# Kernel tuning notes

Hardware: AMD Instinct MI355X
Metric: run time of the kernel (lower is better)

The kernel has to match this reference:

```python
import jax, jax.numpy as jnp
import numpy as np

B, L, H, M = 8, 512, 768, 383
N = M + 1  # +1 dummy epsilon mention
NEG = -10000.0


def _lin(x, W, b):
    return x @ W.T + b


def setup_inputs() -> dict:
    key = jax.random.key(0)
    ks = jax.random.split(key, 26)
    s = 0.02
    inp = {}
    inp["sequence_output"] = jax.random.normal(ks[0], (B, L, H), jnp.float32)
    inp["speaker_emb"] = jax.random.normal(ks[1], (400, H), jnp.float32) * s
    inp["dummy_emb"] = jax.random.normal(ks[2], (1, H), jnp.float32) * s
    inp["W_pair1"] = jax.random.normal(ks[3], (H, 2 * H), jnp.float32) * s
    inp["b_pair1"] = jnp.zeros((H,), jnp.float32)
    inp["W_pair2"] = jax.random.normal(ks[4], (H // 2, H), jnp.float32) * s
    inp["b_pair2"] = jnp.zeros((H // 2,), jnp.float32)
    inp["W_pair3"] = jax.random.normal(ks[5], (1, H // 2), jnp.float32) * s
    inp["b_pair3"] = jnp.zeros((1,), jnp.float32)
    inp["W_m1"] = jax.random.normal(ks[6], (H // 2, H), jnp.float32) * s
    inp["b_m1"] = jnp.zeros((H // 2,), jnp.float32)
    inp["W_m2"] = jax.random.normal(ks[7], (H // 4, H // 2), jnp.float32) * s
    inp["b_m2"] = jnp.zeros((H // 4,), jnp.float32)
    inp["W_m3"] = jax.random.normal(ks[8], (1, H // 4), jnp.float32) * s
    inp["b_m3"] = jnp.zeros((1,), jnp.float32)
    inp["W_c1"] = jax.random.normal(ks[9], (H // 2, H), jnp.float32) * s
    inp["b_c1"] = jnp.zeros((H // 2,), jnp.float32)
    inp["W_c2"] = jax.random.normal(ks[10], (18, H // 2), jnp.float32) * s
    inp["b_c2"] = jnp.zeros((18,), jnp.float32)
    inp["mentions_seg"] = jax.random.randint(ks[11], (M,), 0, B, jnp.int32)
    inp["mention_start"] = jax.random.randint(ks[12], (M,), 0, L, jnp.int32)
    inp["mention_end"] = jax.random.randint(ks[13], (M,), 0, L, jnp.int32)
    inp["speaker_ids"] = jax.random.randint(ks[14], (B, L), 0, 400, jnp.int32)
    second = jnp.arange(1, N, dtype=jnp.int32)  # each real mention is a 'second' exactly once
    first = jax.random.randint(ks[15], (M,), 0, N, jnp.int32) % second  # antecedent strictly before
    inp["link_first"] = first
    inp["link_second"] = second
    inp["character_label"] = jax.random.randint(ks[16], (M,), 0, 18, jnp.int32)
    return inp


def reference(sequence_output, speaker_emb, dummy_emb,
              W_pair1, b_pair1, W_pair2, b_pair2, W_pair3, b_pair3,
              W_m1, b_m1, W_m2, b_m2, W_m3, b_m3,
              W_c1, b_c1, W_c2, b_c2,
              mentions_seg, mention_start, mention_end, speaker_ids,
              link_first, link_second, character_label):
    relu = jax.nn.relu
    # gather mention boundary + speaker reps: [M, H]
    start_rep = sequence_output[mentions_seg, mention_start]
    end_rep = sequence_output[mentions_seg, mention_end]
    spk_rep = speaker_emb[speaker_ids[mentions_seg, mention_start]]
    mention_reps = start_rep + end_rep + spk_rep
    # character linking head: [M, 18]
    char_logits = _lin(relu(_lin(mention_reps, W_c1, b_c1)), W_c2, b_c2)
    # prepend dummy epsilon mention: [N, H]
    all_reps = jnp.concatenate([dummy_emb, mention_reps], axis=0)
    # pairwise MLP; pair[i, j] = MLP(cat(rep_j, rep_i)). Split W_pair1 to avoid [N,N,2H] concat.
    Wa, Wb = W_pair1[:, :H], W_pair1[:, H:]
    A = all_reps @ Wa.T  # contribution of 'first' (column j)
    Bm = all_reps @ Wb.T  # contribution of 'second' (row i)
    h1 = relu(A[None, :, :] + Bm[:, None, :] + b_pair1)  # [N, N, H]
    h2 = relu(jnp.einsum('ijk,hk->ijh', h1, W_pair2) + b_pair2)  # [N, N, H/2]
    pair_scores = jnp.einsum('ijh,oh->ij', h2, W_pair3) + b_pair3[0]  # [N, N]
    # unary mention score: [N]
    ms = (_lin(relu(_lin(relu(_lin(all_reps, W_m1, b_m1)), W_m2, b_m2)), W_m3, b_m3))[:, 0]
    mask = jnp.triu(jnp.ones((N, N), jnp.float32), k=0) * NEG
    mention_scores = pair_scores + ms[None, :] + ms[:, None] + mask
    # linking loss via row-softmax and link gathers
    sm = jax.nn.softmax(mention_scores, axis=1)
    lik = sm[link_second, link_first]  # [num_links]
    col_sum = jnp.zeros((N,), sm.dtype).at[link_second].add(lik)
    nll = -jnp.sum(jnp.log(col_sum[1:]))
    # character cross-entropy (sum reduction)
    logp = jax.nn.log_softmax(char_logits, axis=1)
    ce = -jnp.sum(jnp.take_along_axis(logp, character_label[:, None], axis=1))
    return nll + ce


if __name__ == '__main__':
    out = reference(**setup_inputs())
    print(out)
```

## Files before the change

### kernel.cpp

```cpp
#include <hip/hip_runtime.h>

typedef __bf16 bf16x8 __attribute__((ext_vector_type(8)));
typedef float f32x4 __attribute__((ext_vector_type(4)));

#define WS_ALLREPS 0
#define WS_APRIME  294912
#define WS_BMAT    589824
#define WS_RELUM1  884736
#define WS_RELUC1  1032192
#define WS_MS      1179648
#define WS_W2BF    1180032
#define WS_S       1327488

#define SWZ(row,c) (((row)<<2) + ((c) ^ (((row)>>1)&3)))

__device__ __forceinline__ bf16x8 cvt8(float4 a, float4 b) {
  bf16x8 v;
  v[0]=(__bf16)a.x; v[1]=(__bf16)a.y; v[2]=(__bf16)a.z; v[3]=(__bf16)a.w;
  v[4]=(__bf16)b.x; v[5]=(__bf16)b.y; v[6]=(__bf16)b.z; v[7]=(__bf16)b.w;
  return v;
}

__global__ __launch_bounds__(256) void k_build(
    const float* __restrict__ seq, const float* __restrict__ spk_emb,
    const float* __restrict__ dummy, const float* __restrict__ W2,
    const int* __restrict__ seg, const int* __restrict__ mstart,
    const int* __restrict__ mend, const int* __restrict__ spk_ids,
    float* __restrict__ all_reps, __bf16* __restrict__ W2bf,
    float* __restrict__ out) {
  int r = blockIdx.x, t = threadIdx.x;
  if (r < 384) {
    if (r == 0) {
      if (t == 0) out[0] = 0.f;
      #pragma unroll
      for (int e = 0; e < 3; ++e) { int k = t + 256*e; all_reps[k] = dummy[k]; }
    } else {
      int m = r - 1;
      int sg = seg[m], st = mstart[m], en = mend[m];
      int sp = spk_ids[sg*512 + st];
      const float* p1 = seq + (size_t)(sg*512 + st)*768;
      const float* p2 = seq + (size_t)(sg*512 + en)*768;
      const float* p3 = spk_emb + (size_t)sp*768;
      #pragma unroll
      for (int e = 0; e < 3; ++e) { int k = t + 256*e; all_reps[r*768+k] = p1[k]+p2[k]+p3[k]; }
    }
  } else {
    int h = r - 384;
    #pragma unroll
    for (int e = 0; e < 3; ++e) { int k = t + 256*e; W2bf[h*768+k] = (__bf16)W2[h*768+k]; }
  }
}

__global__ __launch_bounds__(256) void k_gemmB(
    const float* __restrict__ reps, const float* __restrict__ W1,
    const float* __restrict__ Wm1, const float* __restrict__ Wc1,
    const float* __restrict__ b1, const float* __restrict__ bm1, const float* __restrict__ bc1,
    float* __restrict__ Aprime, float* __restrict__ Bmat,
    float* __restrict__ relu_m1, float* __restrict__ relu_c1) {
  __shared__ bf16x8 lA[2][256];
  __shared__ bf16x8 lB[2][512];
  int nt = blockIdx.x;
  int m0 = blockIdx.y * 64;
  int t = threadIdx.x;
  const float* src; int stride, coloff;
  if (nt < 6)       { src = W1  + (size_t)(nt*128)*1536;      stride = 1536; coloff = 0;   }
  else if (nt < 12) { src = W1  + (size_t)((nt-6)*128)*1536;  stride = 1536; coloff = 768; }
  else if (nt < 15) { src = Wm1 + (size_t)((nt-12)*128)*768;  stride = 768;  coloff = 0;   }
  else              { src = Wc1 + (size_t)((nt-15)*128)*768;  stride = 768;  coloff = 0;   }

  int w = t>>6, l = t&63;
  int wm = w&1, wn = w>>1;
  int lr = l&15, lg = l>>4;

  int p = t>>2, q = t&3;
  const float* pa  = reps + (size_t)(m0+p)*768 + q*8;
  const float* pb0 = src + (size_t)p*stride + coloff + q*8;
  const float* pb1 = src + (size_t)(p+64)*stride + coloff + q*8;
  int ia  = SWZ(p, q);
  int ib0 = SWZ(p, q);
  int ib1 = SWZ(p+64, q);

  float4 a0, a1, b0, b1v, c0, c1v;
  #define G_LOADG(k0) { \
    a0  = *(const float4*)(pa  + (k0)); a1  = *(const float4*)(pa  + (k0) + 4); \
    b0  = *(const float4*)(pb0 + (k0)); b1v = *(const float4*)(pb0 + (k0) + 4); \
    c0  = *(const float4*)(pb1 + (k0)); c1v = *(const float4*)(pb1 + (k0) + 4); }
  #define G_WRITEB(buf) { \
    lA[buf][ia]  = cvt8(a0, a1); \
    lB[buf][ib0] = cvt8(b0, b1v); \
    lB[buf][ib1] = cvt8(c0, c1v); }

  G_LOADG(0);
  G_WRITEB(0);

  f32x4 acc[2][4] = {};
  int cur = 0;

  for (int ks = 0; ks < 24; ++ks) {
    __syncthreads();
    if (ks < 23) G_LOADG((ks+1)*32);
    bf16x8 af[2], bfr[4];
    #pragma unroll
    for (int fa = 0; fa < 2; ++fa) { int row = wm*32 + fa*16 + lr; af[fa] = lA[cur][SWZ(row, lg)]; }
    #pragma unroll
    for (int fb = 0; fb < 4; ++fb) { int row = wn*64 + fb*16 + lr; bfr[fb] = lB[cur][SWZ(row, lg)]; }
    __builtin_amdgcn_s_setprio(1);
    #pragma unroll
    for (int fa = 0; fa < 2; ++fa)
      #pragma unroll
      for (int fb = 0; fb < 4; ++fb)
        acc[fa][fb] = __builtin_amdgcn_mfma_f32_16x16x32_bf16(af[fa], bfr[fb], acc[fa][fb], 0, 0, 0);
    __builtin_amdgcn_s_setprio(0);
    if (ks < 23) G_WRITEB(cur^1);
    cur ^= 1;
  }

  #pragma unroll
  for (int fa = 0; fa < 2; ++fa) {
    #pragma unroll
    for (int fb = 0; fb < 4; ++fb) {
      #pragma unroll
      for (int reg = 0; reg < 4; ++reg) {
        int m = m0 + wm*32 + fa*16 + lg*4 + reg;
        int nl = wn*64 + fb*16 + lr;
        float v = acc[fa][fb][reg];
        if (nt < 6)       { int n = nt*128 + nl;      Aprime[m*768+n]  = v + b1[n]; }
        else if (nt < 12) { int n = (nt-6)*128 + nl;  Bmat[m*768+n]    = v; }
        else if (nt < 15) { int n = (nt-12)*128 + nl; relu_m1[m*384+n] = fmaxf(v + bm1[n], 0.f); }
        else              { int n = (nt-15)*128 + nl; relu_c1[m*384+n] = fmaxf(v + bc1[n], 0.f); }
      }
    }
  }
}

__global__ __launch_bounds__(192) void k_ms(
    const float* __restrict__ relu_m1, const float* __restrict__ Wm2,
    const float* __restrict__ bm2, const float* __restrict__ Wm3,
    const float* __restrict__ bm3, float* __restrict__ ms) {
  __shared__ float x[2][384];
  __shared__ float part[2][3];
  int r0 = blockIdx.x*2, t = threadIdx.x;
  const float4* srcv = (const float4*)(relu_m1 + (size_t)r0*384);
  float4* dstv = (float4*)&x[0][0];
  dstv[t] = srcv[t];
  __syncthreads();
  float a[2] = {};
  const float4* wv = (const float4*)(Wm2 + (size_t)t*384);
  for (int k = 0; k < 96; ++k) {
    float4 wq = wv[k];
    #pragma unroll
    for (int r = 0; r < 2; ++r) {
      float4 xq = *(const float4*)&x[r][k*4];
      a[r] += wq.x*xq.x + wq.y*xq.y + wq.z*xq.z + wq.w*xq.w;
    }
  }
  float wm3 = Wm3[t], bb = bm2[t];
  #pragma unroll
  for (int r = 0; r < 2; ++r) {
    float c = fmaxf(a[r] + bb, 0.f) * wm3;
    c += __shfl_xor(c, 1);  c += __shfl_xor(c, 2);  c += __shfl_xor(c, 4);
    c += __shfl_xor(c, 8);  c += __shfl_xor(c, 16); c += __shfl_xor(c, 32);
    if ((t&63) == 0) part[r][t>>6] = c;
  }
  __syncthreads();
  if (t < 2) ms[r0+t] = part[t][0] + part[t][1] + part[t][2] + bm3[0];
}

__global__ __launch_bounds__(256, 2) void k_pair(
    const float* __restrict__ Aprime, const float* __restrict__ Bmat,
    const __bf16* __restrict__ W2bf, const float* __restrict__ b2,
    const float* __restrict__ w3,
    float* __restrict__ S) {
  int bid = blockIdx.x;
  int hh = blockIdx.y;
  int h0 = hh * 192;
  int ib = (int)((__fsqrt_rn(4.0f*bid + 1.0f) - 1.0f) * 0.5f);
  while ((ib+1)*(ib+2) <= bid) ++ib;
  while (ib*(ib+1) > bid) --ib;
  int jb = bid - ib*(ib+1);
  int i0 = ib*16, j0 = jb*8;

  __shared__ bf16x8 lA[2][512];
  __shared__ bf16x8 lB[2][768];
  __shared__ float score_lds[128][2];

  int t = threadIdx.x;
  int w = t>>6, l = t&63;
  int wp = w&1, wh = w>>1;
  int lr = l&15, lg = l>>4;

  int p = t>>1, qb = (t&1)*2;
  const float* pArow = Aprime + (size_t)(j0 + (p&7))*768 + qb*8;
  const float* pBrow = Bmat   + (size_t)(i0 + (p>>3))*768 + qb*8;
  int idxA0 = SWZ(p, qb), idxA1 = SWZ(p, qb+1);
  const __bf16* pW[3]; int idxW[3];
  #pragma unroll
  for (int e = 0; e < 3; ++e) {
    int c = t + 256*e, row = c>>2, qq = c&3;
    pW[e] = W2bf + (size_t)(h0 + row)*768 + qq*8;
    idxW[e] = SWZ(row, qq);
  }

  float4 ga0, ga1, ga2, ga3, gb0, gb1, gb2, gb3;
  bf16x8 gw0, gw1, gw2;

  #define LOADG(k0) { \
    ga0 = *(const float4*)(pArow + (k0));     ga1 = *(const float4*)(pArow + (k0) + 4); \
    ga2 = *(const float4*)(pArow + (k0) + 8); ga3 = *(const float4*)(pArow + (k0) + 12); \
    gb0 = *(const float4*)(pBrow + (k0));     gb1 = *(const float4*)(pBrow + (k0) + 4); \
    gb2 = *(const float4*)(pBrow + (k0) + 8); gb3 = *(const float4*)(pBrow + (k0) + 12); \
    gw0 = *(const bf16x8*)(pW[0] + (k0)); \
    gw1 = *(const bf16x8*)(pW[1] + (k0)); \
    gw2 = *(const bf16x8*)(pW[2] + (k0)); }

  #define WRITEB(buf) { \
    float4 r0, r1, r2, r3; \
    r0.x = fmaxf(ga0.x + gb0.x, 0.f); r0.y = fmaxf(ga0.y + gb0.y, 0.f); \
    r0.z = fmaxf(ga0.z + gb0.z, 0.f); r0.w = fmaxf(ga0.w + gb0.w, 0.f); \
    r1.x = fmaxf(ga1.x + gb1.x, 0.f); r1.y = fmaxf(ga1.y + gb1.y, 0.f); \
    r1.z = fmaxf(ga1.z + gb1.z, 0.f); r1.w = fmaxf(ga1.w + gb1.w, 0.f); \
    r2.x = fmaxf(ga2.x + gb2.x, 0.f); r2.y = fmaxf(ga2.y + gb2.y, 0.f); \
    r2.z = fmaxf(ga2.z + gb2.z, 0.f); r2.w = fmaxf(ga2.w + gb2.w, 0.f); \
    r3.x = fmaxf(ga3.x + gb3.x, 0.f); r3.y = fmaxf(ga3.y + gb3.y, 0.f); \
    r3.z = fmaxf(ga3.z + gb3.z, 0.f); r3.w = fmaxf(ga3.w + gb3.w, 0.f); \
    lA[buf][idxA0] = cvt8(r0, r1); \
    lA[buf][idxA1] = cvt8(r2, r3); \
    lB[buf][idxW[0]] = gw0; lB[buf][idxW[1]] = gw1; lB[buf][idxW[2]] = gw2; }

  LOADG(0);
  WRITEB(0);

  f32x4 acc[4][6] = {};
  int cur = 0;

  for (int ks = 0; ks < 24; ++ks) {
    __syncthreads();
    if (ks < 23) LOADG((ks+1)*32);
    bf16x8 af[4], bfr[6];
    #pragma unroll
    for (int fp = 0; fp < 4; ++fp) { int row = wp*64 + fp*16 + lr; af[fp] = lA[cur][SWZ(row, lg)]; }
    #pragma unroll
    for (int fh = 0; fh < 6; ++fh) { int row = wh*96 + fh*16 + lr; bfr[fh] = lB[cur][SWZ(row, lg)]; }
    __builtin_amdgcn_s_setprio(1);
    #pragma unroll
    for (int fp = 0; fp < 4; ++fp)
      #pragma unroll
      for (int fh = 0; fh < 6; ++fh)
        acc[fp][fh] = __builtin_amdgcn_mfma_f32_16x16x32_bf16(af[fp], bfr[fh], acc[fp][fh], 0, 0, 0);
    __builtin_amdgcn_s_setprio(0);
    if (ks < 23) WRITEB(cur^1);
    cur ^= 1;
  }

  float sacc[4][4] = {};
  #pragma unroll
  for (int fh = 0; fh < 6; ++fh) {
    int hcol = h0 + wh*96 + fh*16 + lr;
    float bb = b2[hcol], ww = w3[hcol];
    #pragma unroll
    for (int fp = 0; fp < 4; ++fp)
      #pragma unroll
      for (int reg = 0; reg < 4; ++reg)
        sacc[fp][reg] += fmaxf(acc[fp][fh][reg] + bb, 0.f) * ww;
  }
  #pragma unroll
  for (int fp = 0; fp < 4; ++fp) {
    #pragma unroll
    for (int reg = 0; reg < 4; ++reg) {
      float v = sacc[fp][reg];
      v += __shfl_xor(v, 1); v += __shfl_xor(v, 2);
      v += __shfl_xor(v, 4); v += __shfl_xor(v, 8);
      if (lr == 0) score_lds[wp*64 + fp*16 + lg*4 + reg][wh] = v;
    }
  }
  __syncthreads();
  if (t < 128) {
    S[(size_t)hh*76800 + bid*128 + t] = score_lds[t][0] + score_lds[t][1];
  }
}

__global__ __launch_bounds__(64) void k_ce(
    const float* __restrict__ relu_c1, const float* __restrict__ Wc2,
    const float* __restrict__ bc2, const int* __restrict__ label,
    float* __restrict__ out) {
  __shared__ float lg[18];
  int m = blockIdx.x, t = threadIdx.x;
  if (t < 18) {
    const float4* xv = (const float4*)(relu_c1 + (size_t)(m+1)*384);
    const float4* wv = (const float4*)(Wc2 + (size_t)t*384);
    float d = 0.f;
    for (int k = 0; k < 96; ++k) {
      float4 a = xv[k], b = wv[k];
      d += a.x*b.x + a.y*b.y + a.z*b.z + a.w*b.w;
    }
    lg[t] = d + bc2[t];
  }
  __syncthreads();
  if (t == 0) {
    float sum = 0.f;
    for (int c = 0; c < 18; ++c) sum += __expf(lg[c]);
    atomicAdd(out, __logf(sum) - lg[label[m]]);
  }
}

__global__ __launch_bounds__(64) void k_epi(
    const float* __restrict__ S, const float* __restrict__ ms,
    const float* __restrict__ b3, const int* __restrict__ lfirst,
    float* __restrict__ out) {
  int i = blockIdx.x + 1;
  int lane = threadIdx.x;
  int ibb = i >> 4, r = i & 15;
  int f = lfirst[i-1];
  float bb3 = b3[0];
  float esum = 0.f, smf = 0.f;
  for (int j = lane; j < i; j += 64) {
    int jbb = j >> 3;
    int idx = (ibb*(ibb+1) + jbb)*128 + r*8 + (j&7);
    float s = S[idx] + S[76800 + idx] + bb3 + ms[j];
    esum += __expf(s);
    if (j == f) smf = s;
  }
  esum += __shfl_xor(esum, 1);  esum += __shfl_xor(esum, 2);
  esum += __shfl_xor(esum, 4);  esum += __shfl_xor(esum, 8);
  esum += __shfl_xor(esum, 16); esum += __shfl_xor(esum, 32);
  smf += __shfl_xor(smf, 1);  smf += __shfl_xor(smf, 2);
  smf += __shfl_xor(smf, 4);  smf += __shfl_xor(smf, 8);
  smf += __shfl_xor(smf, 16); smf += __shfl_xor(smf, 32);
  if (lane == 0) atomicAdd(out, __logf(esum) - smf);
}

extern "C" void kernel_launch(void* const* d_in, const int* in_sizes, int n_in,
                              void* d_out, int out_size, void* d_ws, size_t ws_size,
                              hipStream_t stream) {
  (void)in_sizes; (void)n_in; (void)out_size; (void)ws_size;
  const float* seq   = (const float*)d_in[0];
  const float* spk   = (const float*)d_in[1];
  const float* dummy = (const float*)d_in[2];
  const float* W1    = (const float*)d_in[3];
  const float* b1    = (const float*)d_in[4];
  const float* W2    = (const float*)d_in[5];
  const float* b2    = (const float*)d_in[6];
  const float* W3    = (const float*)d_in[7];
  const float* b3    = (const float*)d_in[8];
  const float* Wm1   = (const float*)d_in[9];
  const float* bm1   = (const float*)d_in[10];
  const float* Wm2   = (const float*)d_in[11];
  const float* bm2   = (const float*)d_in[12];
  const float* Wm3   = (const float*)d_in[13];
  const float* bm3   = (const float*)d_in[14];
  const float* Wc1   = (const float*)d_in[15];
  const float* bc1   = (const float*)d_in[16];
  const float* Wc2   = (const float*)d_in[17];
  const float* bc2   = (const float*)d_in[18];
  const int* seg     = (const int*)d_in[19];
  const int* mstart  = (const int*)d_in[20];
  const int* mend    = (const int*)d_in[21];
  const int* spk_ids = (const int*)d_in[22];
  const int* lfirst  = (const int*)d_in[23];
  const int* clabel  = (const int*)d_in[25];

  float* ws = (float*)d_ws;
  float* all_reps = ws + WS_ALLREPS;
  float* Aprime   = ws + WS_APRIME;
  float* Bmat     = ws + WS_BMAT;
  float* relu_m1  = ws + WS_RELUM1;
  float* relu_c1  = ws + WS_RELUC1;
  float* msv      = ws + WS_MS;
  __bf16* W2bf    = (__bf16*)(ws + WS_W2BF);
  float* S        = ws + WS_S;
  float* out      = (float*)d_out;

  k_build<<<768, 256, 0, stream>>>(seq, spk, dummy, W2, seg, mstart, mend, spk_ids, all_reps, W2bf, out);
  k_gemmB<<<dim3(18,6), 256, 0, stream>>>(all_reps, W1, Wm1, Wc1, b1, bm1, bc1, Aprime, Bmat, relu_m1, relu_c1);
  k_ms<<<192, 192, 0, stream>>>(relu_m1, Wm2, bm2, Wm3, bm3, msv);
  k_pair<<<dim3(600,2), 256, 0, stream>>>(Aprime, Bmat, W2bf, b2, W3, S);
  k_ce<<<383, 64, 0, stream>>>(relu_c1, Wc2, bc2, clabel, out);
  k_epi<<<383, 64, 0, stream>>>(S, msv, b3, lfirst, out);
}
```

Before: 246.8 us.

## Fuse pair, mention-score and CE kernels into one launch with finer triangular tiles

Merges the pairwise MLP, unary mention score and character CE kernels into a single heterogeneous launch dispatched by block index. The pair tiles shrink from 16x8 to 8x8 pairs, so the triangular region is covered more tightly with less wasted upper-triangle work, and each block uses 128 threads. Each wave writes its partial scores to a separate slab, which removes the LDS reduction and barrier but makes the epilogue sum four slabs. The workspace layout is rearranged so S starts at offset 0 and overlaps all_reps, which is safe only because all_reps is dead by then. The cost is more blocks, each redoing more W2 loads per tile.

```diff
diff --git a/kernel.cpp b/kernel.cpp
--- a/kernel.cpp
+++ b/kernel.cpp
@@ -3,14 +3,19 @@
 typedef __bf16 bf16x8 __attribute__((ext_vector_type(8)));
 typedef float f32x4 __attribute__((ext_vector_type(4)));
 
+#define WS_S       0
 #define WS_ALLREPS 0
-#define WS_APRIME  294912
-#define WS_BMAT    589824
-#define WS_RELUM1  884736
-#define WS_RELUC1  1032192
-#define WS_MS      1179648
-#define WS_W2BF    1180032
-#define WS_S       1327488
+#define WS_APRIME  301056
+#define WS_BMAT    595968
+#define WS_RELUM1  890880
+#define WS_RELUC1  1038336
+#define WS_MS      1185792
+#define WS_W2BF    1186176
+
+#define NPAIR 2352
+#define NMS   384
+#define NCE   383
+#define SLAB  75264
 
 #define SWZ(row,c) (((row)<<2) + ((c) ^ (((row)>>1)&3)))
 
@@ -133,173 +138,164 @@
   }
 }
 
-__global__ __launch_bounds__(192) void k_ms(
+__global__ __launch_bounds__(128, 2) void k_mega(
+    const float* __restrict__ Aprime, const float* __restrict__ Bmat,
+    const __bf16* __restrict__ W2bf, const float* __restrict__ b2,
+    const float* __restrict__ w3, float* __restrict__ S,
     const float* __restrict__ relu_m1, const float* __restrict__ Wm2,
     const float* __restrict__ bm2, const float* __restrict__ Wm3,
-    const float* __restrict__ bm3, float* __restrict__ ms) {
-  __shared__ float x[2][384];
-  __shared__ float part[2][3];
-  int r0 = blockIdx.x*2, t = threadIdx.x;
-  const float4* srcv = (const float4*)(relu_m1 + (size_t)r0*384);
-  float4* dstv = (float4*)&x[0][0];
-  dstv[t] = srcv[t];
-  __syncthreads();
-  float a[2] = {};
-  const float4* wv = (const float4*)(Wm2 + (size_t)t*384);
-  for (int k = 0; k < 96; ++k) {
-    float4 wq = wv[k];
-    #pragma unroll
-    for (int r = 0; r < 2; ++r) {
-      float4 xq = *(const float4*)&x[r][k*4];
-      a[r] += wq.x*xq.x + wq.y*xq.y + wq.z*xq.z + wq.w*xq.w;
-    }
-  }
-  float wm3 = Wm3[t], bb = bm2[t];
-  #pragma unroll
-  for (int r = 0; r < 2; ++r) {
-    float c = fmaxf(a[r] + bb, 0.f) * wm3;
-    c += __shfl_xor(c, 1);  c += __shfl_xor(c, 2);  c += __shfl_xor(c, 4);
-    c += __shfl_xor(c, 8);  c += __shfl_xor(c, 16); c += __shfl_xor(c, 32);
-    if ((t&63) == 0) part[r][t>>6] = c;
-  }
-  __syncthreads();
-  if (t < 2) ms[r0+t] = part[t][0] + part[t][1] + part[t][2] + bm3[0];
-}
-
-__global__ __launch_bounds__(256, 2) void k_pair(
-    const float* __restrict__ Aprime, const float* __restrict__ Bmat,
-    const __bf16* __restrict__ W2bf, const float* __restrict__ b2,
-    const float* __restrict__ w3,
-    float* __restrict__ S) {
-  int bid = blockIdx.x;
-  int hh = blockIdx.y;
-  int h0 = hh * 192;
-  int ib = (int)((__fsqrt_rn(4.0f*bid + 1.0f) - 1.0f) * 0.5f);
-  while ((ib+1)*(ib+2) <= bid) ++ib;
-  while (ib*(ib+1) > bid) --ib;
-  int jb = bid - ib*(ib+1);
-  int i0 = ib*16, j0 = jb*8;
-
-  __shared__ bf16x8 lA[2][512];
-  __shared__ bf16x8 lB[2][768];
-  __shared__ float score_lds[128][2];
-
-  int t = threadIdx.x;
-  int w = t>>6, l = t&63;
-  int wp = w&1, wh = w>>1;
-  int lr = l&15, lg = l>>4;
-
-  int p = t>>1, qb = (t&1)*2;
-  const float* pArow = Aprime + (size_t)(j0 + (p&7))*768 + qb*8;
-  const float* pBrow = Bmat   + (size_t)(i0 + (p>>3))*768 + qb*8;
-  int idxA0 = SWZ(p, qb), idxA1 = SWZ(p, qb+1);
-  const __bf16* pW[3]; int idxW[3];
-  #pragma unroll
-  for (int e = 0; e < 3; ++e) {
-    int c = t + 256*e, row = c>>2, qq = c&3;
-    pW[e] = W2bf + (size_t)(h0 + row)*768 + qq*8;
-    idxW[e] = SWZ(row, qq);
-  }
-
-  float4 ga0, ga1, ga2, ga3, gb0, gb1, gb2, gb3;
-  bf16x8 gw0, gw1, gw2;
-
-  #define LOADG(k0) { \
-    ga0 = *(const float4*)(pArow + (k0));     ga1 = *(const float4*)(pArow + (k0) + 4); \
-    ga2 = *(const float4*)(pArow + (k0) + 8); ga3 = *(const float4*)(pArow + (k0) + 12); \
-    gb0 = *(const float4*)(pBrow + (k0));     gb1 = *(const float4*)(pBrow + (k0) + 4); \
-    gb2 = *(const float4*)(pBrow + (k0) + 8); gb3 = *(const float4*)(pBrow + (k0) + 12); \
-    gw0 = *(const bf16x8*)(pW[0] + (k0)); \
-    gw1 = *(const bf16x8*)(pW[1] + (k0)); \
-    gw2 = *(const bf16x8*)(pW[2] + (k0)); }
-
-  #define WRITEB(buf) { \
-    float4 r0, r1, r2, r3; \
-    r0.x = fmaxf(ga0.x + gb0.x, 0.f); r0.y = fmaxf(ga0.y + gb0.y, 0.f); \
-    r0.z = fmaxf(ga0.z + gb0.z, 0.f); r0.w = fmaxf(ga0.w + gb0.w, 0.f); \
-    r1.x = fmaxf(ga1.x + gb1.x, 0.f); r1.y = fmaxf(ga1.y + gb1.y, 0.f); \
-    r1.z = fmaxf(ga1.z + gb1.z, 0.f); r1.w = fmaxf(ga1.w + gb1.w, 0.f); \
-    r2.x = fmaxf(ga2.x + gb2.x, 0.f); r2.y = fmaxf(ga2.y + gb2.y, 0.f); \
-    r2.z = fmaxf(ga2.z + gb2.z, 0.f); r2.w = fmaxf(ga2.w + gb2.w, 0.f); \
-    r3.x = fmaxf(ga3.x + gb3.x, 0.f); r3.y = fmaxf(ga3.y + gb3.y, 0.f); \
-    r3.z = fmaxf(ga3.z + gb3.z, 0.f); r3.w = fmaxf(ga3.w + gb3.w, 0.f); \
-    lA[buf][idxA0] = cvt8(r0, r1); \
-    lA[buf][idxA1] = cvt8(r2, r3); \
-    lB[buf][idxW[0]] = gw0; lB[buf][idxW[1]] = gw1; lB[buf][idxW[2]] = gw2; }
-
-  LOADG(0);
-  WRITEB(0);
-
-  f32x4 acc[4][6] = {};
-  int cur = 0;
-
-  for (int ks = 0; ks < 24; ++ks) {
-    __syncthreads();
-    if (ks < 23) LOADG((ks+1)*32);
-    bf16x8 af[4], bfr[6];
-    #pragma unroll
-    for (int fp = 0; fp < 4; ++fp) { int row = wp*64 + fp*16 + lr; af[fp] = lA[cur][SWZ(row, lg)]; }
-    #pragma unroll
-    for (int fh = 0; fh < 6; ++fh) { int row = wh*96 + fh*16 + lr; bfr[fh] = lB[cur][SWZ(row, lg)]; }
-    __builtin_amdgcn_s_setprio(1);
-    #pragma unroll
-    for (int fp = 0; fp < 4; ++fp)
-      #pragma unroll
-      for (int fh = 0; fh < 6; ++fh)
-        acc[fp][fh] = __builtin_amdgcn_mfma_f32_16x16x32_bf16(af[fp], bfr[fh], acc[fp][fh], 0, 0, 0);
-    __builtin_amdgcn_s_setprio(0);
-    if (ks < 23) WRITEB(cur^1);
-    cur ^= 1;
-  }
-
-  float sacc[4][4] = {};
-  #pragma unroll
-  for (int fh = 0; fh < 6; ++fh) {
-    int hcol = h0 + wh*96 + fh*16 + lr;
-    float bb = b2[hcol], ww = w3[hcol];
-    #pragma unroll
-    for (int fp = 0; fp < 4; ++fp)
-      #pragma unroll
-      for (int reg = 0; reg < 4; ++reg)
-        sacc[fp][reg] += fmaxf(acc[fp][fh][reg] + bb, 0.f) * ww;
-  }
-  #pragma unroll
-  for (int fp = 0; fp < 4; ++fp) {
-    #pragma unroll
-    for (int reg = 0; reg < 4; ++reg) {
-      float v = sacc[fp][reg];
-      v += __shfl_xor(v, 1); v += __shfl_xor(v, 2);
-      v += __shfl_xor(v, 4); v += __shfl_xor(v, 8);
-      if (lr == 0) score_lds[wp*64 + fp*16 + lg*4 + reg][wh] = v;
-    }
-  }
-  __syncthreads();
-  if (t < 128) {
-    S[(size_t)hh*76800 + bid*128 + t] = score_lds[t][0] + score_lds[t][1];
-  }
-}
-
-__global__ __launch_bounds__(64) void k_ce(
+    const float* __restrict__ bm3, float* __restrict__ msv,
     const float* __restrict__ relu_c1, const float* __restrict__ Wc2,
     const float* __restrict__ bc2, const int* __restrict__ label,
     float* __restrict__ out) {
-  __shared__ float lg[18];
-  int m = blockIdx.x, t = threadIdx.x;
-  if (t < 18) {
-    const float4* xv = (const float4*)(relu_c1 + (size_t)(m+1)*384);
-    const float4* wv = (const float4*)(Wc2 + (size_t)t*384);
-    float d = 0.f;
+  __shared__ char smem[32768];
+  int bx = blockIdx.x, t = threadIdx.x;
+
+  if (bx < NPAIR) {
+    bf16x8 (*lA)[256] = (bf16x8 (*)[256])smem;
+    bf16x8 (*lB)[768] = (bf16x8 (*)[768])(smem + 8192);
+    int tile = bx >> 1, hh = bx & 1;
+    int ib = (int)((__fsqrt_rn(8.0f*tile + 1.0f) - 1.0f) * 0.5f);
+    while ((ib+1)*(ib+2)/2 <= tile) ++ib;
+    while (ib*(ib+1)/2 > tile) --ib;
+    int jb = tile - ib*(ib+1)/2;
+    int i0 = ib*8, j0 = jb*8;
+    int h0 = hh*192;
+
+    int w = t>>6, l = t&63;
+    int lr = l&15, lg = l>>4;
+
+    int p = t>>1, qb = (t&1)*2;
+    const float* pArow = Aprime + (size_t)(j0 + (p&7))*768 + qb*8;
+    const float* pBrow = Bmat   + (size_t)(i0 + (p>>3))*768 + qb*8;
+    int idxA0 = SWZ(p, qb), idxA1 = SWZ(p, qb+1);
+    const __bf16* pW[6]; int idxW[6];
+    #pragma unroll
+    for (int e = 0; e < 6; ++e) {
+      int c6 = t + 128*e, row = c6>>2, qq = c6&3;
+      pW[e] = W2bf + (size_t)(h0 + row)*768 + qq*8;
+      idxW[e] = SWZ(row, qq);
+    }
+
+    float4 ga0, ga1, ga2, ga3, gb0, gb1, gb2, gb3;
+    bf16x8 gw0, gw1, gw2, gw3, gw4, gw5;
+
+    #define LOADG(k0) { \
+      ga0 = *(const float4*)(pArow + (k0));     ga1 = *(const float4*)(pArow + (k0) + 4); \
+      ga2 = *(const float4*)(pArow + (k0) + 8); ga3 = *(const float4*)(pArow + (k0) + 12); \
+      gb0 = *(const float4*)(pBrow + (k0));     gb1 = *(const float4*)(pBrow + (k0) + 4); \
+      gb2 = *(const float4*)(pBrow + (k0) + 8); gb3 = *(const float4*)(pBrow + (k0) + 12); \
+      gw0 = *(const bf16x8*)(pW[0] + (k0)); gw1 = *(const bf16x8*)(pW[1] + (k0)); \
+      gw2 = *(const bf16x8*)(pW[2] + (k0)); gw3 = *(const bf16x8*)(pW[3] + (k0)); \
+      gw4 = *(const bf16x8*)(pW[4] + (k0)); gw5 = *(const bf16x8*)(pW[5] + (k0)); }
+
+    #define WRITEB(buf) { \
+      float4 r0, r1, r2, r3; \
+      r0.x = fmaxf(ga0.x + gb0.x, 0.f); r0.y = fmaxf(ga0.y + gb0.y, 0.f); \
+      r0.z = fmaxf(ga0.z + gb0.z, 0.f); r0.w = fmaxf(ga0.w + gb0.w, 0.f); \
+      r1.x = fmaxf(ga1.x + gb1.x, 0.f); r1.y = fmaxf(ga1.y + gb1.y, 0.f); \
+      r1.z = fmaxf(ga1.z + gb1.z, 0.f); r1.w = fmaxf(ga1.w + gb1.w, 0.f); \
+      r2.x = fmaxf(ga2.x + gb2.x, 0.f); r2.y = fmaxf(ga2.y + gb2.y, 0.f); \
+      r2.z = fmaxf(ga2.z + gb2.z, 0.f); r2.w = fmaxf(ga2.w + gb2.w, 0.f); \
+      r3.x = fmaxf(ga3.x + gb3.x, 0.f); r3.y = fmaxf(ga3.y + gb3.y, 0.f); \
+      r3.z = fmaxf(ga3.z + gb3.z, 0.f); r3.w = fmaxf(ga3.w + gb3.w, 0.f); \
+      lA[buf][idxA0] = cvt8(r0, r1); \
+      lA[buf][idxA1] = cvt8(r2, r3); \
+      lB[buf][idxW[0]] = gw0; lB[buf][idxW[1]] = gw1; lB[buf][idxW[2]] = gw2; \
+      lB[buf][idxW[3]] = gw3; lB[buf][idxW[4]] = gw4; lB[buf][idxW[5]] = gw5; }
+
+    LOADG(0);
+    WRITEB(0);
+
+    f32x4 acc[4][6] = {};
+    int cur = 0;
+
+    for (int ks = 0; ks < 24; ++ks) {
+      __syncthreads();
+      if (ks < 23) LOADG((ks+1)*32);
+      bf16x8 af[4], bfr[6];
+      #pragma unroll
+      for (int fp = 0; fp < 4; ++fp) { int row = fp*16 + lr; af[fp] = lA[cur][SWZ(row, lg)]; }
+      #pragma unroll
+      for (int fh = 0; fh < 6; ++fh) { int row = w*96 + fh*16 + lr; bfr[fh] = lB[cur][SWZ(row, lg)]; }
+      __builtin_amdgcn_s_setprio(1);
+      #pragma unroll
+      for (int fp = 0; fp < 4; ++fp)
+        #pragma unroll
+        for (int fh = 0; fh < 6; ++fh)
+          acc[fp][fh] = __builtin_amdgcn_mfma_f32_16x16x32_bf16(af[fp], bfr[fh], acc[fp][fh], 0, 0, 0);
+      __builtin_amdgcn_s_setprio(0);
+      if (ks < 23) WRITEB(cur^1);
+      cur ^= 1;
+    }
+
+    float sacc[4][4] = {};
+    #pragma unroll
+    for (int fh = 0; fh < 6; ++fh) {
+      int hcol = h0 + w*96 + fh*16 + lr;
+      float bb = b2[hcol], ww = w3[hcol];
+      #pragma unroll
+      for (int fp = 0; fp < 4; ++fp)
+        #pragma unroll
+        for (int reg = 0; reg < 4; ++reg)
+          sacc[fp][reg] += fmaxf(acc[fp][fh][reg] + bb, 0.f) * ww;
+    }
+    float* Sp = S + (size_t)(hh*2 + w)*SLAB + tile*64;
+    #pragma unroll
+    for (int fp = 0; fp < 4; ++fp) {
+      #pragma unroll
+      for (int reg = 0; reg < 4; ++reg) {
+        float v = sacc[fp][reg];
+        v += __shfl_xor(v, 1); v += __shfl_xor(v, 2);
+        v += __shfl_xor(v, 4); v += __shfl_xor(v, 8);
+        if (lr == 0) Sp[fp*16 + lg*4 + reg] = v;
+      }
+    }
+  } else if (bx < NPAIR + NMS) {
+    float* xs = (float*)smem;
+    __shared__ float part[2];
+    int r = bx - NPAIR;
+    const float4* srcv = (const float4*)(relu_m1 + (size_t)r*384);
+    if (t < 96) ((float4*)xs)[t] = srcv[t];
+    __syncthreads();
+    float d1 = 0.f, d2 = 0.f;
+    const float4* w1v = (const float4*)(Wm2 + (size_t)t*384);
+    const float4* w2v = (const float4*)(Wm2 + (size_t)(t+128 < 192 ? t+128 : t)*384);
     for (int k = 0; k < 96; ++k) {
-      float4 a = xv[k], b = wv[k];
-      d += a.x*b.x + a.y*b.y + a.z*b.z + a.w*b.w;
-    }
-    lg[t] = d + bc2[t];
-  }
-  __syncthreads();
-  if (t == 0) {
-    float sum = 0.f;
-    for (int c = 0; c < 18; ++c) sum += __expf(lg[c]);
-    atomicAdd(out, __logf(sum) - lg[label[m]]);
+      float4 xq = ((const float4*)xs)[k];
+      float4 aq = w1v[k];
+      d1 += aq.x*xq.x + aq.y*xq.y + aq.z*xq.z + aq.w*xq.w;
+      if (t < 64) {
+        float4 bq = w2v[k];
+        d2 += bq.x*xq.x + bq.y*xq.y + bq.z*xq.z + bq.w*xq.w;
+      }
+    }
+    float c = fmaxf(d1 + bm2[t], 0.f) * Wm3[t];
+    if (t < 64) c += fmaxf(d2 + bm2[t+128], 0.f) * Wm3[t+128];
+    c += __shfl_xor(c, 1);  c += __shfl_xor(c, 2);  c += __shfl_xor(c, 4);
+    c += __shfl_xor(c, 8);  c += __shfl_xor(c, 16); c += __shfl_xor(c, 32);
+    if ((t&63) == 0) part[t>>6] = c;
+    __syncthreads();
+    if (t == 0) msv[r] = part[0] + part[1] + bm3[0];
+  } else {
+    float* lg = (float*)smem;
+    int m = bx - (NPAIR + NMS);
+    if (t < 18) {
+      const float4* xv = (const float4*)(relu_c1 + (size_t)(m+1)*384);
+      const float4* wv = (const float4*)(Wc2 + (size_t)t*384);
+      float d = 0.f;
+      for (int k = 0; k < 96; ++k) {
+        float4 a = xv[k], b = wv[k];
+        d += a.x*b.x + a.y*b.y + a.z*b.z + a.w*b.w;
+      }
+      lg[t] = d + bc2[t];
+    }
+    __syncthreads();
+    if (t == 0) {
+      float sum = 0.f;
+      for (int c = 0; c < 18; ++c) sum += __expf(lg[c]);
+      atomicAdd(out, __logf(sum) - lg[label[m]]);
+    }
   }
 }
 
@@ -309,14 +305,15 @@
     float* __restrict__ out) {
   int i = blockIdx.x + 1;
   int lane = threadIdx.x;
-  int ibb = i >> 4, r = i & 15;
+  int ibb = i >> 3, r = i & 7;
   int f = lfirst[i-1];
   float bb3 = b3[0];
   float esum = 0.f, smf = 0.f;
+  int tri = ibb*(ibb+1)/2;
   for (int j = lane; j < i; j += 64) {
     int jbb = j >> 3;
-    int idx = (ibb*(ibb+1) + jbb)*128 + r*8 + (j&7);
-    float s = S[idx] + S[76800 + idx] + bb3 + ms[j];
+    int idx = (tri + jbb)*64 + r*8 + (j&7);
+    float s = S[idx] + S[SLAB + idx] + S[2*SLAB + idx] + S[3*SLAB + idx] + bb3 + ms[j];
     esum += __expf(s);
     if (j == f) smf = s;
   }
@@ -360,6 +357,7 @@
   const int* clabel  = (const int*)d_in[25];
 
   float* ws = (float*)d_ws;
+  float* S        = ws + WS_S;
   float* all_reps = ws + WS_ALLREPS;
   float* Aprime   = ws + WS_APRIME;
   float* Bmat     = ws + WS_BMAT;
@@ -367,13 +365,12 @@
   float* relu_c1  = ws + WS_RELUC1;
   float* msv      = ws + WS_MS;
   __bf16* W2bf    = (__bf16*)(ws + WS_W2BF);
-  float* S        = ws + WS_S;
   float* out      = (float*)d_out;
 
   k_build<<<768, 256, 0, stream>>>(seq, spk, dummy, W2, seg, mstart, mend, spk_ids, all_reps, W2bf, out);
   k_gemmB<<<dim3(18,6), 256, 0, stream>>>(all_reps, W1, Wm1, Wc1, b1, bm1, bc1, Aprime, Bmat, relu_m1, relu_c1);
-  k_ms<<<192, 192, 0, stream>>>(relu_m1, Wm2, bm2, Wm3, bm3, msv);
-  k_pair<<<dim3(600,2), 256, 0, stream>>>(Aprime, Bmat, W2bf, b2, W3, S);
-  k_ce<<<383, 64, 0, stream>>>(relu_c1, Wc2, bc2, clabel, out);
+  k_mega<<<NPAIR + NMS + NCE, 128, 0, stream>>>(Aprime, Bmat, W2bf, b2, W3, S,
+                                                relu_m1, Wm2, bm2, Wm3, bm3, msv,
+                                                relu_c1, Wc2, bc2, clabel, out);
   k_epi<<<383, 64, 0, stream>>>(S, msv, b3, lfirst, out);
 }
```

Result: faster. 240.2 us (-2.7%).
